# Kernel optimization log

Measured on AMD Instinct MI355X. Metric: run time of the kernel, lower is better.

The kernel has to match this reference:

```python
import jax, jax.numpy as jnp
import numpy as np

NUM_SAMPLES = 4096
TAU = 0.07
EPS = 1e-20


def setup_inputs() -> dict:
    key = jax.random.key(0)
    flows = jax.random.normal(key, (32, 2, 512, 512), dtype=jnp.float32)
    return {"flows": flows}


def reference(flows):
    # flows: [b, 2, h, w]
    b, _, h, w = flows.shape
    hw = h * w
    # sampling weights: L2 norm over the 2 flow components, scaled by 1/tau
    dist = jnp.sqrt(jnp.sum(flows * flows, axis=1)) / TAU  # [b, h, w]
    dist = dist.reshape(b, hw)  # [b, h*w]
    # torch.multinomial(dist, k) without replacement == Gumbel-top-k on log-weights
    logits = jnp.log(dist + EPS)
    g = jax.random.gumbel(jax.random.key(42), (b, hw), dtype=flows.dtype)
    _, indices = jax.lax.top_k(logits + g, NUM_SAMPLES)  # [b, num_samples] int32
    # scatter-based mask (equivalent to one_hot(indices).max(dim=1), without the
    # huge [b, num_samples, h*w] intermediate)
    batch_idx = jnp.arange(b)[:, None]  # [b, 1]
    flat_masks = jnp.zeros((b, hw), dtype=flows.dtype).at[batch_idx, indices].set(1.0)
    masks = flat_masks.reshape(b, 1, h, w)  # [b, 1, h, w]
    sparse_output = masks * flows  # [b, 2, h, w]
    sparse_output = jnp.concatenate([sparse_output, masks], axis=1)  # [b, 3, h, w]
    return sparse_output, indices, masks
```

## Files before the change

### kernel.cpp

```cpp
#include <hip/hip_runtime.h>
#include <stdint.h>

#define HW 262144
#define NB 32
#define TOPK 4096
#define NTOTAL (NB * HW)
#define GBLK 4096
#define CBLK 32768

#define OUT_F4 8421376u
#define GTHREADS 524288u

typedef float f32x4 __attribute__((ext_vector_type(4)));

#define OFF_WIN 33554432
#define OFF_HA  35651584
#define OFF_HB  37748736
#define OFF_STA 39845888
#define OFF_STT 39846144
#define OFF_FLG 39846272
#define OFF_CNT 39846400

__device__ __forceinline__ uint32_t rotl32(uint32_t x, int d) {
  return (x << d) | (x >> (32 - d));
}

__device__ __forceinline__ void threefry2x32_k42(uint32_t x0, uint32_t x1,
                                                 uint32_t& o0, uint32_t& o1) {
  const uint32_t ks0 = 0u;
  const uint32_t ks1 = 42u;
  const uint32_t ks2 = 0x1BD11BDAu ^ 0u ^ 42u;
  x0 += ks0;
  x1 += ks1;
#define TF_ROUND(r) { x0 += x1; x1 = rotl32(x1, (r)); x1 ^= x0; }
  TF_ROUND(13) TF_ROUND(15) TF_ROUND(26) TF_ROUND(6)
  x0 += ks1; x1 += ks2 + 1u;
  TF_ROUND(17) TF_ROUND(29) TF_ROUND(16) TF_ROUND(24)
  x0 += ks2; x1 += ks0 + 2u;
  TF_ROUND(13) TF_ROUND(15) TF_ROUND(26) TF_ROUND(6)
  x0 += ks0; x1 += ks1 + 3u;
  TF_ROUND(17) TF_ROUND(29) TF_ROUND(16) TF_ROUND(24)
  x0 += ks1; x1 += ks2 + 4u;
  TF_ROUND(13) TF_ROUND(15) TF_ROUND(26) TF_ROUND(6)
  x0 += ks2; x1 += ks0 + 5u;
#undef TF_ROUND
  o0 = x0;
  o1 = x1;
}

__device__ __forceinline__ float eigen_plogf(float xin) {
#pragma clang fp contract(off)
  uint32_t ux = __float_as_uint(xin);
  int e_int = (int)(ux >> 23) - 126;
  float x = __uint_as_float((ux & 0x007fffffu) | 0x3f000000u);
  float e = (float)e_int;
  const float SQRTHF = 0.707106781186547524f;
  bool m = (x < SQRTHF);
  float tmp = m ? x : 0.0f;
  x = x - 1.0f;
  e = e - (m ? 1.0f : 0.0f);
  x = x + tmp;
  float x2 = x * x;
  float x3 = x2 * x;
  float y  = fmaf(7.0376836292e-2f,  x, -1.1514610310e-1f);
  float y1 = fmaf(-1.2420140846e-1f, x,  1.4249322787e-1f);
  float y2 = fmaf(2.0000714765e-1f,  x, -2.4999993993e-1f);
  y  = fmaf(y,  x,  1.1676998740e-1f);
  y1 = fmaf(y1, x, -1.6668057665e-1f);
  y2 = fmaf(y2, x,  3.3333331174e-1f);
  y  = fmaf(y,  x3, y1);
  y  = fmaf(y,  x3, y2);
  y  = y * x3;
  float ey1 = e * -2.12194440e-4f;
  float t2  = x2 * 0.5f;
  y = y + ey1;
  x = x - t2;
  float ey2 = e * 0.693359375f;
  x = x + y;
  x = x + ey2;
  return x;
}

__device__ __forceinline__ float np_logf(float xin) {
#pragma clang fp contract(off)
  uint32_t ux = __float_as_uint(xin);
  int e2 = (int)(ux >> 23) - 127;
  float mant = __uint_as_float((ux & 0x007fffffu) | 0x3f800000u);
  if (mant >= 1.5f) { mant = mant * 0.5f; e2 += 1; }
  float e = (float)e2;
  float t = mant - 1.0f;
  float num = fmaf(2.589979117907922693523e-02f, t, 3.808837741388407920751e-01f);
  num = fmaf(num, t, 1.480000633400055983228e+00f);
  num = fmaf(num, t, 2.112677543073053063722e+00f);
  num = fmaf(num, t, 9.999999999999998702752e-01f);
  num = num * t;
  float den = fmaf(5.875095403124574342950e-03f, t, 1.546476374983906719538e-01f);
  den = fmaf(den, t, 9.864942958519418960339e-01f);
  den = fmaf(den, t, 2.453006071784736363091e+00f);
  den = fmaf(den, t, 2.612677543073109236779e+00f);
  den = fmaf(den, t, 1.0f);
  float r = num / den;
  return fmaf(e, 0.693147182464599609375f, r);
}

__device__ __forceinline__ uint32_t order_key(const float* __restrict__ flows,
                                              int p, uint32_t bits) {
#pragma clang fp contract(off)
  int b = p >> 18;
  int j = p & (HW - 1);
  const float* fb = flows + ((size_t)b << 19);
  float x = fb[j];
  float y = fb[j + HW];
  float xx = x * x;
  float yy = y * y;
  float ss = xx + yy;
  float sq = (float)sqrt((double)ss);
  float dist = (float)((double)sq / (double)0.07f);
  float logits = np_logf(dist + 1e-20f);
  float f = __uint_as_float((bits >> 9) | 0x3f800000u) - 1.0f;
  float u = fmaxf(f, 1.17549435e-38f);
  float g = -eigen_plogf(-eigen_plogf(u));
  float s = logits + g;
  uint32_t mm = __float_as_uint(s);
  mm = (mm & 0x80000000u) ? ~mm : (mm | 0x80000000u);
  return ~mm;
}

__global__ __launch_bounds__(1024) void k_compute(const float* __restrict__ flows,
                                                  uint32_t* __restrict__ d,
                                                  uint32_t* __restrict__ histA) {
  __shared__ uint32_t lh[8192];
  for (int i = threadIdx.x; i < 8192; i += 1024) lh[i] = 0u;
  __syncthreads();
  int base = blockIdx.x * CBLK;
  int b = base >> 18;
  for (int it = 0; it < CBLK / 1024; ++it) {
    int p = base + it * 1024 + threadIdx.x;
    uint32_t o0, o1;
    threefry2x32_k42(0u, (uint32_t)p, o0, o1);
    uint32_t dv = order_key(flows, p, o0 ^ o1);
    d[p] = dv;
    atomicAdd(&lh[dv >> 19], 1u);
  }
  __syncthreads();
  uint32_t* hb = histA + ((uint32_t)b << 13);
  for (int i = threadIdx.x; i < 8192; i += 1024) {
    uint32_t c = lh[i];
    if (c) atomicAdd(&hb[i], c);
  }
}

__global__ __launch_bounds__(1024) void k_scanAB(const uint32_t* __restrict__ histA,
                                                 const uint32_t* __restrict__ d,
                                                 uint32_t* __restrict__ histB,
                                                 uint32_t* __restrict__ stateA,
                                                 uint32_t* __restrict__ stateT,
                                                 uint32_t* __restrict__ flag) {
  __shared__ uint32_t ls[1024];
  __shared__ uint32_t bc[3];
  int b = blockIdx.x;
  {
    const uint32_t* h = histA + ((uint32_t)b << 13);
    int base = threadIdx.x * 8;
    uint32_t s = 0;
    for (int i = 0; i < 8; ++i) s += h[base + i];
    ls[threadIdx.x] = s;
    __syncthreads();
    for (int off = 1; off < 1024; off <<= 1) {
      uint32_t v = (threadIdx.x >= off) ? ls[threadIdx.x - off] : 0u;
      __syncthreads();
      ls[threadIdx.x] += v;
      __syncthreads();
    }
    uint32_t incl = ls[threadIdx.x];
    uint32_t excl = incl - s;
    if (excl < TOPK && TOPK <= incl) {
      uint32_t cum = excl;
      for (int i = 0; i < 8; ++i) {
        uint32_t c = h[base + i];
        if (cum + c >= TOPK) {
          uint32_t B = (uint32_t)(base + i);
          stateA[2 * b] = B;
          stateA[2 * b + 1] = TOPK - cum;
          stateT[b] = (B << 19) | 0x7FFFFu;
          uint32_t ov = (cum + c > 8192u) ? 1u : 0u;
          flag[b] = ov;
          bc[0] = B; bc[1] = TOPK - cum; bc[2] = ov;
          break;
        }
        cum += c;
      }
    }
  }
  __syncthreads();
  if (bc[2] == 0u) return;
  uint32_t B = bc[0];
  uint32_t target = bc[1];
  uint32_t* h2 = histB + ((uint32_t)b << 14);
  const uint32_t* db = d + ((size_t)b << 18);
  for (int it = 0; it < HW / 1024; ++it) {
    uint32_t dv = db[it * 1024 + threadIdx.x];
    if ((dv >> 19) == B)
      atomicAdd(&h2[(dv >> 5) & 0x3FFFu], 1u);
  }
  __threadfence();
  __syncthreads();
  {
    int base = threadIdx.x * 16;
    uint32_t s = 0;
    for (int i = 0; i < 16; ++i) s += h2[base + i];
    ls[threadIdx.x] = s;
    __syncthreads();
    for (int off = 1; off < 1024; off <<= 1) {
      uint32_t v = (threadIdx.x >= off) ? ls[threadIdx.x - off] : 0u;
      __syncthreads();
      ls[threadIdx.x] += v;
      __syncthreads();
    }
    uint32_t incl = ls[threadIdx.x];
    uint32_t excl = incl - s;
    if (excl < target && target <= incl) {
      uint32_t cum = excl;
      for (int i = 0; i < 16; ++i) {
        uint32_t c = h2[base + i];
        if (cum + c >= target) {
          stateT[b] = (B << 19) | ((uint32_t)(base + i) << 5) | 0x1Fu;
          break;
        }
        cum += c;
      }
    }
  }
}

__global__ __launch_bounds__(256) void k_gather(const uint32_t* __restrict__ d,
                                                const uint32_t* __restrict__ stateT,
                                                uint32_t* __restrict__ cnt,
                                                unsigned long long* __restrict__ winners,
                                                f32x4* __restrict__ outz) {
  __shared__ unsigned long long buf[GBLK];
  __shared__ uint32_t lcnt;
  __shared__ uint32_t gbase;
  int base = blockIdx.x * GBLK;
  int b = base >> 18;
  uint32_t T = stateT[b];
  uint32_t gt = (uint32_t)blockIdx.x * 256u + threadIdx.x;
  const f32x4 z4 = {0.f, 0.f, 0.f, 0.f};
  if (threadIdx.x == 0) lcnt = 0u;
  __syncthreads();
  for (int it = 0; it < GBLK / 256; ++it) {
    int p = base + it * 256 + threadIdx.x;
    uint32_t dv = d[p];
    outz[(uint32_t)it * GTHREADS + gt] = z4;
    if (dv <= T) {
      uint32_t pos = atomicAdd(&lcnt, 1u);
      buf[pos] = ((unsigned long long)dv << 32) |
                 (unsigned long long)(p & (HW - 1));
    }
  }
  { uint32_t z = 16u * GTHREADS + gt;
    if (z < OUT_F4) outz[z] = z4; }
  __syncthreads();
  uint32_t n = lcnt;
  if (threadIdx.x == 0 && n) gbase = atomicAdd(&cnt[b], n);
  __syncthreads();
  for (uint32_t i = threadIdx.x; i < n; i += 256) {
    uint32_t pos = gbase + i;
    if (pos < 8192u) winners[(size_t)b * 8192 + pos] = buf[i];
  }
}

__global__ __launch_bounds__(1024) void k_sort1(const uint32_t* __restrict__ cnt,
                                                unsigned long long* __restrict__ winners) {
  __shared__ unsigned long long s[1024];
  int blk = blockIdx.x;
  int b = blk >> 3;
  int c = blk & 7;
  uint32_t n = cnt[b];
  if (n > 8192u) n = 8192u;
  int goff = b * 8192 + c * 1024;
  int t = threadIdx.x;
  s[t] = ((uint32_t)(c * 1024 + t) < n) ? winners[goff + t]
                                        : 0xFFFFFFFFFFFFFFFFull;
  __syncthreads();
  for (int k = 2; k <= 1024; k <<= 1) {
    for (int j = k >> 1; j > 0; j >>= 1) {
      int ixj = t ^ j;
      if (ixj > t) {
        bool up = ((t & k) == 0);
        unsigned long long a = s[t];
        unsigned long long cc = s[ixj];
        if ((a > cc) == up) { s[t] = cc; s[ixj] = a; }
      }
      __syncthreads();
    }
  }
  winners[goff + t] = s[t];
}

__global__ __launch_bounds__(1024) void k_rank(const unsigned long long* __restrict__ winners,
                                               const float* __restrict__ flows,
                                               float* __restrict__ out0,
                                               float* __restrict__ out_idx,
                                               float* __restrict__ out_masks) {
  __shared__ unsigned long long s[8192];
  int b = blockIdx.x >> 3;
  int part = blockIdx.x & 7;
  for (int i = threadIdx.x; i < 8192; i += 1024)
    s[i] = winners[(size_t)b * 8192 + i];
  __syncthreads();
  const float* fb = flows + ((size_t)b << 19);
  int i = (part << 10) + threadIdx.x;
  unsigned long long w = s[i];
  if (w != 0xFFFFFFFFFFFFFFFFull) {
    int rank = threadIdx.x;
    for (int c = 0; c < 8; ++c) {
      if (c == part) continue;
      int lo = 0, hi = 1024;
      while (lo < hi) {
        int mid = (lo + hi) >> 1;
        if (s[(c << 10) + mid] < w) lo = mid + 1; else hi = mid;
      }
      rank += lo;
    }
    if (rank < TOPK) {
      uint32_t idx = (uint32_t)(w & 0xFFFFFFFFull);
      out_idx[(size_t)b * TOPK + rank] = (float)idx;
      float x = fb[idx];
      float y = fb[idx + HW];
      size_t o = ((size_t)b * 3) * HW + idx;
      out0[o] = x;
      out0[o + HW] = y;
      out0[o + 2 * HW] = 1.0f;
      out_masks[(size_t)b * HW + idx] = 1.0f;
    }
  }
}

extern "C" void kernel_launch(void* const* d_in, const int* in_sizes, int n_in,
                              void* d_out, int out_size, void* d_ws, size_t ws_size,
                              hipStream_t stream) {
  const float* flows = (const float*)d_in[0];
  float* out = (float*)d_out;
  char* ws = (char*)d_ws;

  uint32_t* d = (uint32_t*)ws;
  unsigned long long* winners = (unsigned long long*)(ws + OFF_WIN);
  uint32_t* histA = (uint32_t*)(ws + OFF_HA);
  uint32_t* histB = (uint32_t*)(ws + OFF_HB);
  uint32_t* stateA = (uint32_t*)(ws + OFF_STA);
  uint32_t* stateT = (uint32_t*)(ws + OFF_STT);
  uint32_t* flag = (uint32_t*)(ws + OFF_FLG);
  uint32_t* cnt = (uint32_t*)(ws + OFF_CNT);

  float* out_idx = out + (size_t)NB * 3 * HW;
  float* out_masks = out_idx + (size_t)NB * TOPK;

  (void)hipMemsetAsync(ws + OFF_HA, 0, 4194304 + 1024, stream);

  k_compute<<<NTOTAL / CBLK, 1024, 0, stream>>>(flows, d, histA);
  k_scanAB<<<NB, 1024, 0, stream>>>(histA, d, histB, stateA, stateT, flag);
  k_gather<<<NTOTAL / GBLK, 256, 0, stream>>>(d, stateT, cnt, winners,
                                              (f32x4*)out);
  k_sort1<<<NB * 8, 1024, 0, stream>>>(cnt, winners);
  k_rank<<<NB * 8, 1024, 0, stream>>>(winners, flows, out, out_idx, out_masks);
}
```

Before: 295.9 us.

## Replace global atomic histograms with per-block partials and shared-memory refine histogram

Each compute block now writes its private 8192-bin histogram as uint16 partials instead of atomically accumulating into a zeroed global histogram. The scan kernel sums the 8 partials per batch, and the second-level refinement histogram moves from global memory into 64KB of shared memory. This removes the 4MB memset launch and the global atomics, and the per-batch counter is now zeroed inside the scan kernel. In exchange the scan kernel reads more data, and the large shared allocation may limit occupancy, though it runs only 32 blocks anyway.

```diff
diff --git a/kernel.cpp b/kernel.cpp
--- a/kernel.cpp
+++ b/kernel.cpp
@@ -14,8 +14,7 @@
 typedef float f32x4 __attribute__((ext_vector_type(4)));
 
 #define OFF_WIN 33554432
-#define OFF_HA  35651584
-#define OFF_HB  37748736
+#define OFF_HP  35651584
 #define OFF_STA 39845888
 #define OFF_STT 39846144
 #define OFF_FLG 39846272
@@ -128,12 +127,11 @@
 
 __global__ __launch_bounds__(1024) void k_compute(const float* __restrict__ flows,
                                                   uint32_t* __restrict__ d,
-                                                  uint32_t* __restrict__ histA) {
+                                                  uint16_t* __restrict__ histP) {
   __shared__ uint32_t lh[8192];
   for (int i = threadIdx.x; i < 8192; i += 1024) lh[i] = 0u;
   __syncthreads();
   int base = blockIdx.x * CBLK;
-  int b = base >> 18;
   for (int it = 0; it < CBLK / 1024; ++it) {
     int p = base + it * 1024 + threadIdx.x;
     uint32_t o0, o1;
@@ -143,27 +141,35 @@
     atomicAdd(&lh[dv >> 19], 1u);
   }
   __syncthreads();
-  uint32_t* hb = histA + ((uint32_t)b << 13);
-  for (int i = threadIdx.x; i < 8192; i += 1024) {
-    uint32_t c = lh[i];
-    if (c) atomicAdd(&hb[i], c);
-  }
-}
-
-__global__ __launch_bounds__(1024) void k_scanAB(const uint32_t* __restrict__ histA,
+  uint16_t* hb = histP + ((uint32_t)blockIdx.x << 13);
+  for (int i = threadIdx.x; i < 8192; i += 1024)
+    hb[i] = (uint16_t)lh[i];
+}
+
+__global__ __launch_bounds__(1024) void k_scanAB(const uint16_t* __restrict__ histP,
                                                  const uint32_t* __restrict__ d,
-                                                 uint32_t* __restrict__ histB,
                                                  uint32_t* __restrict__ stateA,
                                                  uint32_t* __restrict__ stateT,
-                                                 uint32_t* __restrict__ flag) {
+                                                 uint32_t* __restrict__ flag,
+                                                 uint32_t* __restrict__ cnt) {
   __shared__ uint32_t ls[1024];
+  __shared__ uint32_t lh2[16384];
   __shared__ uint32_t bc[3];
   int b = blockIdx.x;
+  if (threadIdx.x == 0) cnt[b] = 0u;
   {
-    const uint32_t* h = histA + ((uint32_t)b << 13);
+    const uint16_t* hp = histP + ((uint32_t)(b * 8) << 13);
     int base = threadIdx.x * 8;
+    uint32_t bs[8];
     uint32_t s = 0;
-    for (int i = 0; i < 8; ++i) s += h[base + i];
+#pragma unroll
+    for (int i = 0; i < 8; ++i) {
+      uint32_t t = 0;
+#pragma unroll
+      for (int c = 0; c < 8; ++c) t += hp[(c << 13) + base + i];
+      bs[i] = t;
+      s += t;
+    }
     ls[threadIdx.x] = s;
     __syncthreads();
     for (int off = 1; off < 1024; off <<= 1) {
@@ -176,8 +182,9 @@
     uint32_t excl = incl - s;
     if (excl < TOPK && TOPK <= incl) {
       uint32_t cum = excl;
+#pragma unroll
       for (int i = 0; i < 8; ++i) {
-        uint32_t c = h[base + i];
+        uint32_t c = bs[i];
         if (cum + c >= TOPK) {
           uint32_t B = (uint32_t)(base + i);
           stateA[2 * b] = B;
@@ -196,19 +203,19 @@
   if (bc[2] == 0u) return;
   uint32_t B = bc[0];
   uint32_t target = bc[1];
-  uint32_t* h2 = histB + ((uint32_t)b << 14);
+  for (int i = threadIdx.x; i < 16384; i += 1024) lh2[i] = 0u;
+  __syncthreads();
   const uint32_t* db = d + ((size_t)b << 18);
   for (int it = 0; it < HW / 1024; ++it) {
     uint32_t dv = db[it * 1024 + threadIdx.x];
     if ((dv >> 19) == B)
-      atomicAdd(&h2[(dv >> 5) & 0x3FFFu], 1u);
-  }
-  __threadfence();
+      atomicAdd(&lh2[(dv >> 5) & 0x3FFFu], 1u);
+  }
   __syncthreads();
   {
     int base = threadIdx.x * 16;
     uint32_t s = 0;
-    for (int i = 0; i < 16; ++i) s += h2[base + i];
+    for (int i = 0; i < 16; ++i) s += lh2[base + i];
     ls[threadIdx.x] = s;
     __syncthreads();
     for (int off = 1; off < 1024; off <<= 1) {
@@ -222,7 +229,7 @@
     if (excl < target && target <= incl) {
       uint32_t cum = excl;
       for (int i = 0; i < 16; ++i) {
-        uint32_t c = h2[base + i];
+        uint32_t c = lh2[base + i];
         if (cum + c >= target) {
           stateT[b] = (B << 19) | ((uint32_t)(base + i) << 5) | 0x1Fu;
           break;
@@ -346,8 +353,7 @@
 
   uint32_t* d = (uint32_t*)ws;
   unsigned long long* winners = (unsigned long long*)(ws + OFF_WIN);
-  uint32_t* histA = (uint32_t*)(ws + OFF_HA);
-  uint32_t* histB = (uint32_t*)(ws + OFF_HB);
+  uint16_t* histP = (uint16_t*)(ws + OFF_HP);
   uint32_t* stateA = (uint32_t*)(ws + OFF_STA);
   uint32_t* stateT = (uint32_t*)(ws + OFF_STT);
   uint32_t* flag = (uint32_t*)(ws + OFF_FLG);
@@ -356,10 +362,8 @@
   float* out_idx = out + (size_t)NB * 3 * HW;
   float* out_masks = out_idx + (size_t)NB * TOPK;
 
-  (void)hipMemsetAsync(ws + OFF_HA, 0, 4194304 + 1024, stream);
-
-  k_compute<<<NTOTAL / CBLK, 1024, 0, stream>>>(flows, d, histA);
-  k_scanAB<<<NB, 1024, 0, stream>>>(histA, d, histB, stateA, stateT, flag);
+  k_compute<<<NTOTAL / CBLK, 1024, 0, stream>>>(flows, d, histP);
+  k_scanAB<<<NB, 1024, 0, stream>>>(histP, d, stateA, stateT, flag, cnt);
   k_gather<<<NTOTAL / GBLK, 256, 0, stream>>>(d, stateT, cnt, winners,
                                               (f32x4*)out);
   k_sort1<<<NB * 8, 1024, 0, stream>>>(cnt, winners);
```

After: 294.4 us. No clear change (-0.5%).
